# Kernel tuning notes

Hardware: AMD Instinct MI355X
Metric: run time of the kernel (lower is better)

The kernel has to match this reference:

```python
import jax, jax.numpy as jnp
import numpy as np

D = 32          # d_model / gcn channels
H_HEADS = 4
HEAD_D = D // H_HEADS
FF = 2048       # TransformerEncoderLayer default dim_feedforward
NUM_CLASSES = 10
EPS = 1e-5


def setup_inputs() -> dict:
    key = jax.random.key(0)
    ks = jax.random.split(key, 24)
    B, Cin, Hh, Ww = 1024, 16, 4, 8          # H*W == 32 (required by reshape into GCN)
    N = B * D                                 # 32768 graph nodes
    E = 2097152                               # ~avg degree 64
    p = lambda k, shp: (jax.random.normal(k, shp, dtype=jnp.float32) * 0.05)
    return {
        "x": jax.random.normal(ks[0], (B, Cin, Hh, Ww), dtype=jnp.float32),
        "edge_index": jax.random.randint(ks[1], (2, E), 0, N, dtype=jnp.int32),
        "conv_w": p(ks[2], (32, Cin, 3, 3)), "conv_b": p(ks[3], (32,)),
        "in_proj_w": p(ks[4], (3 * D, D)), "in_proj_b": p(ks[5], (3 * D,)),
        "out_proj_w": p(ks[6], (D, D)), "out_proj_b": p(ks[7], (D,)),
        "ln1_w": jnp.ones((D,), jnp.float32), "ln1_b": jnp.zeros((D,), jnp.float32),
        "ln2_w": jnp.ones((D,), jnp.float32), "ln2_b": jnp.zeros((D,), jnp.float32),
        "ff1_w": p(ks[8], (FF, D)), "ff1_b": p(ks[9], (FF,)),
        "ff2_w": p(ks[10], (D, FF)), "ff2_b": p(ks[11], (D,)),
        "gcn_w": p(ks[12], (D, D)), "gcn_b": p(ks[13], (D,)),
        "fc_w": p(ks[14], (NUM_CLASSES, D)), "fc_b": p(ks[15], (NUM_CLASSES,)),
    }


def _layernorm(v, w, b):
    m = v.mean(-1, keepdims=True)
    var = v.var(-1, keepdims=True)
    return (v - m) * jax.lax.rsqrt(var + EPS) * w + b


def _gcn(x, row, col, n, w, b):
    # PyG GCNConv: add self-loops, symmetric D^-1/2 (A+I) D^-1/2, x@W^T, + bias
    deg = jax.ops.segment_sum(jnp.ones(row.shape[0], x.dtype), col, num_segments=n)
    dis = jax.lax.rsqrt(jnp.maximum(deg, 1.0))  # self-loops guarantee deg>=1
    norm = dis[row] * dis[col]
    xw = x @ w.T
    msg = xw[row] * norm[:, None]
    return jax.ops.segment_sum(msg, col, num_segments=n) + b


def reference(x, edge_index, conv_w, conv_b, in_proj_w, in_proj_b, out_proj_w,
              out_proj_b, ln1_w, ln1_b, ln2_w, ln2_b, ff1_w, ff1_b, ff2_w, ff2_b,
              gcn_w, gcn_b, fc_w, fc_b):
    # conv2d, padding=1 stride=1 -> SAME
    h = jax.lax.conv_general_dilated(x, conv_w, (1, 1), "SAME",
                                     dimension_numbers=("NCHW", "OIHW", "NCHW"))
    h = h + conv_b[None, :, None, None]
    B, C, Hh, Ww = h.shape
    z = h.reshape(B, C, Hh * Ww).transpose(0, 2, 1)  # (B, HW, 32)

    # torch TransformerEncoderLayer, batch_first=False: axis0=seq(B), axis1=batch(HW)
    qkv = z @ in_proj_w.T + in_proj_b                 # (S, Nb, 3D)
    q, k, v = jnp.split(qkv, 3, axis=-1)
    S, Nb = z.shape[0], z.shape[1]
    rs = lambda t: t.reshape(S, Nb, H_HEADS, HEAD_D)
    q, k, v = rs(q), rs(k), rs(v)
    scores = jnp.einsum("snhd,tnhd->nhst", q, k) / np.sqrt(HEAD_D).astype(np.float32)
    attn = jax.nn.softmax(scores, axis=-1)
    o = jnp.einsum("nhst,tnhd->snhd", attn, v).reshape(S, Nb, D)
    o = o @ out_proj_w.T + out_proj_b
    z = _layernorm(z + o, ln1_w, ln1_b)               # post-norm (torch default)
    ff = jax.nn.relu(z @ ff1_w.T + ff1_b) @ ff2_w.T + ff2_b
    z = _layernorm(z + ff, ln2_w, ln2_b)

    # (B, HW, 32) -> (B, 32, HW) -> (B*32, HW) ; HW == 32 so GCN in_channels match
    g = z.transpose(0, 2, 1).reshape(B * C, Hh * Ww)
    n = g.shape[0]
    loops = jnp.arange(n, dtype=edge_index.dtype)
    row = jnp.concatenate([edge_index[0], loops])
    col = jnp.concatenate([edge_index[1], loops])
    g = _gcn(g, row, col, n, gcn_w, gcn_b)
    g = jax.nn.relu(g)  # dropout is identity in eval mode
    g = _gcn(g, row, col, n, gcn_w, gcn_b)            # shared weights (same module)
    logits = g @ fc_w.T + fc_b
    return jax.nn.log_softmax(logits, axis=1)
```

## Files before the change

### kernel.cpp

```cpp
#include <hip/hip_runtime.h>

#define NTOK 32768

__global__ __launch_bounds__(256) void conv_kernel(
    const float* __restrict__ x, const float* __restrict__ w,
    const float* __restrict__ bias, float* __restrict__ z) {
  __shared__ float xs[16 * 32];
  __shared__ float wsm[32 * 145];
  __shared__ float bs[32];
  int b = blockIdx.x, tid = threadIdx.x;
  const float* xb = x + b * 512;
  for (int i = tid; i < 512; i += 256) xs[i] = xb[i];
  for (int i = tid; i < 4608; i += 256) wsm[(i / 144) * 145 + (i % 144)] = w[i];
  if (tid < 32) bs[tid] = bias[tid];
  __syncthreads();
  #pragma unroll
  for (int r = 0; r < 4; ++r) {
    int oid = r * 256 + tid;
    int co = oid & 31, pos = oid >> 5;
    int y = pos >> 3, xx = pos & 7;
    float acc = bs[co];
    const float* wr = &wsm[co * 145];
    for (int ci = 0; ci < 16; ++ci) {
      #pragma unroll
      for (int ky = 0; ky < 3; ++ky) {
        int yy = y + ky - 1;
        if (yy < 0 || yy > 3) continue;
        #pragma unroll
        for (int kx = 0; kx < 3; ++kx) {
          int xc = xx + kx - 1;
          if (xc < 0 || xc > 7) continue;
          acc += xs[ci * 32 + yy * 8 + xc] * wr[ci * 9 + ky * 3 + kx];
        }
      }
    }
    z[(b * 32 + pos) * 32 + co] = acc;
  }
}

__global__ __launch_bounds__(256) void qkv_kernel(
    const float* __restrict__ z, const float* __restrict__ W,
    const float* __restrict__ bias, float* __restrict__ qt,
    float* __restrict__ kt, float* __restrict__ vt) {
  __shared__ float wsm[96 * 32];
  __shared__ float bs[96];
  int tid = threadIdx.x;
  for (int i = tid; i < 3072; i += 256) wsm[i] = W[i];
  if (tid < 96) bs[tid] = bias[tid];
  __syncthreads();
  int s = tid >> 3, bl = tid & 7;
  int b = blockIdx.x * 8 + bl;
  int token = b * 32 + s;
  float zr[32];
  const float4* zp = (const float4*)(z + token * 32);
  #pragma unroll
  for (int i = 0; i < 8; ++i) {
    float4 v = zp[i];
    zr[i * 4 + 0] = v.x; zr[i * 4 + 1] = v.y; zr[i * 4 + 2] = v.z; zr[i * 4 + 3] = v.w;
  }
  for (int part = 0; part < 3; ++part) {
    float* dst = part == 0 ? qt : (part == 1 ? kt : vt);
    for (int hh = 0; hh < 4; ++hh) {
      float out[8];
      #pragma unroll
      for (int j = 0; j < 8; ++j) {
        int jj = part * 32 + hh * 8 + j;
        float a = bs[jj];
        const float* wr = &wsm[jj * 32];
        #pragma unroll
        for (int k = 0; k < 32; ++k) a += zr[k] * wr[k];
        out[j] = a;
      }
      float4* p = (float4*)(dst + ((size_t)(s * 4 + hh) * 1024 + b) * 8);
      p[0] = make_float4(out[0], out[1], out[2], out[3]);
      p[1] = make_float4(out[4], out[5], out[6], out[7]);
    }
  }
}

__global__ __launch_bounds__(256) void attn_kernel(
    const float* __restrict__ qt, const float* __restrict__ kt,
    const float* __restrict__ vt, float* __restrict__ o) {
  __shared__ __align__(16) float Ks[1024 * 8];
  __shared__ __align__(16) float Vs[1024 * 8];
  int slab = blockIdx.x >> 2, qc = blockIdx.x & 3;
  int tid = threadIdx.x;
  const float4* kp = (const float4*)(kt + (size_t)slab * 8192);
  const float4* vp = (const float4*)(vt + (size_t)slab * 8192);
  float4* ksp = (float4*)Ks;
  float4* vsp = (float4*)Vs;
  for (int i = tid; i < 2048; i += 256) { ksp[i] = kp[i]; vsp[i] = vp[i]; }
  __syncthreads();
  int b = qc * 256 + tid;
  const float4* qp = (const float4*)(qt + ((size_t)slab * 1024 + b) * 8);
  float4 q0 = qp[0], q1 = qp[1];
  const float scale = 0.35355339059327373f;
  q0.x *= scale; q0.y *= scale; q0.z *= scale; q0.w *= scale;
  q1.x *= scale; q1.y *= scale; q1.z *= scale; q1.w *= scale;
  float m = -1e30f;
  for (int t = 0; t < 1024; ++t) {
    const float4* kk = (const float4*)&Ks[t * 8];
    float4 k0 = kk[0], k1 = kk[1];
    float s = q0.x * k0.x + q0.y * k0.y + q0.z * k0.z + q0.w * k0.w +
              q1.x * k1.x + q1.y * k1.y + q1.z * k1.z + q1.w * k1.w;
    m = fmaxf(m, s);
  }
  float l = 0.f;
  float a0 = 0, a1 = 0, a2 = 0, a3 = 0, a4 = 0, a5 = 0, a6 = 0, a7 = 0;
  for (int t = 0; t < 1024; ++t) {
    const float4* kk = (const float4*)&Ks[t * 8];
    float4 k0 = kk[0], k1 = kk[1];
    float s = q0.x * k0.x + q0.y * k0.y + q0.z * k0.z + q0.w * k0.w +
              q1.x * k1.x + q1.y * k1.y + q1.z * k1.z + q1.w * k1.w;
    float p = __expf(s - m);
    l += p;
    const float4* vv = (const float4*)&Vs[t * 8];
    float4 v0 = vv[0], v1 = vv[1];
    a0 += p * v0.x; a1 += p * v0.y; a2 += p * v0.z; a3 += p * v0.w;
    a4 += p * v1.x; a5 += p * v1.y; a6 += p * v1.z; a7 += p * v1.w;
  }
  float inv = 1.f / l;
  int npos = slab >> 2, hh = slab & 3;
  float4* op = (float4*)(o + ((size_t)(b * 32 + npos)) * 32 + hh * 8);
  op[0] = make_float4(a0 * inv, a1 * inv, a2 * inv, a3 * inv);
  op[1] = make_float4(a4 * inv, a5 * inv, a6 * inv, a7 * inv);
}

__global__ __launch_bounds__(256) void proj_ln1_kernel(
    const float* __restrict__ z, const float* __restrict__ o,
    const float* __restrict__ W, const float* __restrict__ bias,
    const float* __restrict__ lw, const float* __restrict__ lb,
    float* __restrict__ zn1) {
  __shared__ float wsm[1024];
  __shared__ float bs[32], lws[32], lbs[32];
  int tid = threadIdx.x;
  for (int i = tid; i < 1024; i += 256) wsm[i] = W[i];
  if (tid < 32) { bs[tid] = bias[tid]; lws[tid] = lw[tid]; lbs[tid] = lb[tid]; }
  __syncthreads();
  int token = blockIdx.x * 256 + tid;
  float orow[32], zrow[32], v[32];
  const float4* opnt = (const float4*)(o + (size_t)token * 32);
  const float4* zp = (const float4*)(z + (size_t)token * 32);
  #pragma unroll
  for (int i = 0; i < 8; ++i) {
    float4 t4 = opnt[i];
    orow[i * 4] = t4.x; orow[i * 4 + 1] = t4.y; orow[i * 4 + 2] = t4.z; orow[i * 4 + 3] = t4.w;
    float4 z4 = zp[i];
    zrow[i * 4] = z4.x; zrow[i * 4 + 1] = z4.y; zrow[i * 4 + 2] = z4.z; zrow[i * 4 + 3] = z4.w;
  }
  float s1 = 0.f, s2 = 0.f;
  for (int j = 0; j < 32; ++j) {
    float a = bs[j];
    const float* wr = &wsm[j * 32];
    #pragma unroll
    for (int k = 0; k < 32; ++k) a += orow[k] * wr[k];
    float t = a + zrow[j];
    v[j] = t; s1 += t; s2 += t * t;
  }
  float mean = s1 * (1.f / 32.f);
  float var = s2 * (1.f / 32.f) - mean * mean;
  float rs = rsqrtf(var + 1e-5f);
  float4* dst = (float4*)(zn1 + (size_t)token * 32);
  #pragma unroll
  for (int k4 = 0; k4 < 8; ++k4) {
    float4 ov;
    ov.x = (v[k4 * 4 + 0] - mean) * rs * lws[k4 * 4 + 0] + lbs[k4 * 4 + 0];
    ov.y = (v[k4 * 4 + 1] - mean) * rs * lws[k4 * 4 + 1] + lbs[k4 * 4 + 1];
    ov.z = (v[k4 * 4 + 2] - mean) * rs * lws[k4 * 4 + 2] + lbs[k4 * 4 + 2];
    ov.w = (v[k4 * 4 + 3] - mean) * rs * lws[k4 * 4 + 3] + lbs[k4 * 4 + 3];
    dst[k4] = ov;
  }
}

__global__ __launch_bounds__(256, 2) void ffn_kernel(
    const float* __restrict__ zn1, const float* __restrict__ w1,
    const float* __restrict__ b1, const float* __restrict__ w2,
    const float* __restrict__ b2, const float* __restrict__ lw,
    const float* __restrict__ lb, float* __restrict__ zn2) {
  __shared__ __align__(16) float zT[64 * 36];
  __shared__ float w1T[32 * 128];
  __shared__ __align__(16) float w2T[128 * 36];
  __shared__ __align__(16) float hT[64 * 132];
  __shared__ float b1s[128];
  __shared__ float lws[32], lbs[32], b2s[32];
  float* outT = hT;
  int tid = threadIdx.x;
  int t0 = blockIdx.x * 64;
  for (int i = tid; i < 512; i += 256) {
    int rw = i >> 3, c4 = i & 7;
    float4 v = ((const float4*)(zn1 + (size_t)(t0 + rw) * 32))[c4];
    *(float4*)&zT[rw * 36 + c4 * 4] = v;
  }
  if (tid < 32) { lws[tid] = lw[tid]; lbs[tid] = lb[tid]; b2s[tid] = b2[tid]; }
  __syncthreads();
  int tok4 = tid >> 2, dg = tid & 3;
  int f = tid & 127, hi = tid >> 7;
  float acc[8];
  #pragma unroll
  for (int j = 0; j < 8; ++j) acc[j] = b2s[dg * 8 + j];
  for (int ch = 0; ch < 16; ++ch) {
    __syncthreads();
    for (int i = tid; i < 1024; i += 256) {
      int fr = i & 127, k4 = i >> 7;
      float4 v = ((const float4*)(w1 + (size_t)(ch * 128 + fr) * 32))[k4];
      w1T[(k4 * 4 + 0) * 128 + fr] = v.x;
      w1T[(k4 * 4 + 1) * 128 + fr] = v.y;
      w1T[(k4 * 4 + 2) * 128 + fr] = v.z;
      w1T[(k4 * 4 + 3) * 128 + fr] = v.w;
    }
    for (int i = tid; i < 1024; i += 256) {
      int d = i & 31, f4 = i >> 5;
      float4 v = ((const float4*)(w2 + (size_t)d * 2048 + ch * 128))[f4];
      w2T[(f4 * 4 + 0) * 36 + d] = v.x;
      w2T[(f4 * 4 + 1) * 36 + d] = v.y;
      w2T[(f4 * 4 + 2) * 36 + d] = v.z;
      w2T[(f4 * 4 + 3) * 36 + d] = v.w;
    }
    if (tid < 128) b1s[tid] = b1[ch * 128 + tid];
    __syncthreads();
    float w1c[32];
    #pragma unroll
    for (int k = 0; k < 32; ++k) w1c[k] = w1T[k * 128 + f];
    float bb = b1s[f];
    for (int ii = 0; ii < 32; ++ii) {
      int tk = 2 * ii + hi;
      const float4* zr4 = (const float4*)&zT[tk * 36];
      float a = bb;
      #pragma unroll
      for (int k4 = 0; k4 < 8; ++k4) {
        float4 zv = zr4[k4];
        a += zv.x * w1c[k4 * 4] + zv.y * w1c[k4 * 4 + 1] + zv.z * w1c[k4 * 4 + 2] + zv.w * w1c[k4 * 4 + 3];
      }
      hT[tk * 132 + f] = fmaxf(a, 0.f);
    }
    __syncthreads();
    for (int fi = 0; fi < 128; ++fi) {
      float hv = hT[tok4 * 132 + fi];
      const float4* wr = (const float4*)&w2T[fi * 36 + dg * 8];
      float4 x0 = wr[0], x1 = wr[1];
      acc[0] += hv * x0.x; acc[1] += hv * x0.y; acc[2] += hv * x0.z; acc[3] += hv * x0.w;
      acc[4] += hv * x1.x; acc[5] += hv * x1.y; acc[6] += hv * x1.z; acc[7] += hv * x1.w;
    }
  }
  __syncthreads();
  #pragma unroll
  for (int j = 0; j < 8; ++j) outT[tok4 * 33 + dg * 8 + j] = acc[j];
  __syncthreads();
  if (tid < 64) {
    float v[32];
    float s1 = 0.f, s2 = 0.f;
    #pragma unroll
    for (int k = 0; k < 32; ++k) {
      float t = zT[tid * 36 + k] + outT[tid * 33 + k];
      v[k] = t; s1 += t; s2 += t * t;
    }
    float mean = s1 * (1.f / 32.f);
    float var = s2 * (1.f / 32.f) - mean * mean;
    float rs = rsqrtf(var + 1e-5f);
    float4* dst = (float4*)(zn2 + (size_t)(t0 + tid) * 32);
    #pragma unroll
    for (int k4 = 0; k4 < 8; ++k4) {
      float4 ov;
      ov.x = (v[k4 * 4 + 0] - mean) * rs * lws[k4 * 4 + 0] + lbs[k4 * 4 + 0];
      ov.y = (v[k4 * 4 + 1] - mean) * rs * lws[k4 * 4 + 1] + lbs[k4 * 4 + 1];
      ov.z = (v[k4 * 4 + 2] - mean) * rs * lws[k4 * 4 + 2] + lbs[k4 * 4 + 2];
      ov.w = (v[k4 * 4 + 3] - mean) * rs * lws[k4 * 4 + 3] + lbs[k4 * 4 + 3];
      dst[k4] = ov;
    }
  }
}

__global__ __launch_bounds__(256) void transpose_kernel(
    const float* __restrict__ zn2, float* __restrict__ g) {
  __shared__ float t[32 * 33];
  int b = blockIdx.x, tid = threadIdx.x;
  const float* src = zn2 + (size_t)b * 1024;
  #pragma unroll
  for (int l = 0; l < 4; ++l) {
    int o_ = l * 256 + tid;
    t[(o_ >> 5) * 33 + (o_ & 31)] = src[o_];
  }
  __syncthreads();
  float* dst = g + (size_t)b * 1024;
  #pragma unroll
  for (int l = 0; l < 4; ++l) {
    int o_ = l * 256 + tid;
    int c = o_ >> 5, s = o_ & 31;
    dst[o_] = t[s * 33 + c];
  }
}

__global__ void degi_kernel(const int* __restrict__ col, int* __restrict__ degi, int E) {
  int e = blockIdx.x * 256 + threadIdx.x;
  if (e < E) atomicAdd(&degi[col[e]], 1);
}

__global__ __launch_bounds__(1024) void scan_kernel(
    const int* __restrict__ degi, int* __restrict__ offs, int* __restrict__ cur,
    float* __restrict__ dis, int E) {
  __shared__ int ts[1024];
  int tid = threadIdx.x;
  int base = tid * 32;
  int loc[32];
  int s = 0;
  #pragma unroll
  for (int i = 0; i < 32; ++i) { loc[i] = s; s += degi[base + i]; }
  ts[tid] = s;
  __syncthreads();
  for (int d = 1; d < 1024; d <<= 1) {
    int v = (tid >= d) ? ts[tid - d] : 0;
    __syncthreads();
    ts[tid] += v;
    __syncthreads();
  }
  int excl = (tid == 0) ? 0 : ts[tid - 1];
  #pragma unroll
  for (int i = 0; i < 32; ++i) {
    int o = excl + loc[i];
    offs[base + i] = o;
    cur[base + i] = o;
    dis[base + i] = rsqrtf((float)(degi[base + i] + 1));
  }
  if (tid == 1023) offs[NTOK] = E;
}

__global__ void fill_kernel(const int* __restrict__ row, const int* __restrict__ col,
                            const float* __restrict__ dis, int* __restrict__ cur,
                            int2* __restrict__ erec, int E) {
  int e = blockIdx.x * 256 + threadIdx.x;
  if (e >= E) return;
  int r = row[e], c = col[e];
  int slot = atomicAdd(&cur[c], 1);
  float nrm = dis[r] * dis[c];
  erec[slot] = make_int2(r, __float_as_int(nrm));
}

__global__ __launch_bounds__(256) void gcn_in_kernel(
    const float* __restrict__ g, const float* __restrict__ w,
    float* __restrict__ xw) {
  __shared__ float wsm[1024];
  int tid = threadIdx.x;
  for (int i = tid; i < 1024; i += 256) wsm[i] = w[i];
  __syncthreads();
  int n = blockIdx.x * 256 + tid;
  float gr[32];
  const float4* gp = (const float4*)(g + (size_t)n * 32);
  #pragma unroll
  for (int i = 0; i < 8; ++i) {
    float4 v = gp[i];
    gr[i * 4] = v.x; gr[i * 4 + 1] = v.y; gr[i * 4 + 2] = v.z; gr[i * 4 + 3] = v.w;
  }
  float4* xp = (float4*)(xw + (size_t)n * 32);
  for (int d4 = 0; d4 < 8; ++d4) {
    float o_[4];
    #pragma unroll
    for (int j = 0; j < 4; ++j) {
      const float* wr = &wsm[(d4 * 4 + j) * 32];
      float a = 0.f;
      #pragma unroll
      for (int k = 0; k < 32; ++k) a += gr[k] * wr[k];
      o_[j] = a;
    }
    xp[d4] = make_float4(o_[0], o_[1], o_[2], o_[3]);
  }
}

__global__ __launch_bounds__(256) void gather_kernel(
    const float* __restrict__ xw, const float* __restrict__ dis,
    const int* __restrict__ offs, const int2* __restrict__ erec,
    float* __restrict__ agg) {
  int gid = blockIdx.x * 256 + threadIdx.x;
  int c = gid >> 3, q = gid & 7;
  int start = offs[c], end = offs[c + 1];
  float dn = dis[c];
  float dn2 = dn * dn;
  float4 self = ((const float4*)(xw + (size_t)c * 32))[q];
  float a0 = self.x * dn2, a1 = self.y * dn2, a2 = self.z * dn2, a3 = self.w * dn2;
  int e = start;
  #pragma unroll 4
  for (; e < end; ++e) {
    int2 rec = erec[e];
    float nrm = __int_as_float(rec.y);
    float4 v = ((const float4*)(xw + (size_t)rec.x * 32))[q];
    a0 += v.x * nrm; a1 += v.y * nrm; a2 += v.z * nrm; a3 += v.w * nrm;
  }
  ((float4*)(agg + (size_t)c * 32))[q] = make_float4(a0, a1, a2, a3);
}

__global__ __launch_bounds__(256) void gcn_mid_kernel(
    const float* __restrict__ agg, const float* __restrict__ gb,
    const float* __restrict__ w, float* __restrict__ xw2) {
  __shared__ float wsm[1024];
  __shared__ float bs[32];
  int tid = threadIdx.x;
  for (int i = tid; i < 1024; i += 256) wsm[i] = w[i];
  if (tid < 32) bs[tid] = gb[tid];
  __syncthreads();
  int n = blockIdx.x * 256 + tid;
  float gr[32];
  const float4* ap = (const float4*)(agg + (size_t)n * 32);
  #pragma unroll
  for (int i = 0; i < 8; ++i) {
    float4 v = ap[i];
    gr[i * 4 + 0] = fmaxf(v.x + bs[i * 4 + 0], 0.f);
    gr[i * 4 + 1] = fmaxf(v.y + bs[i * 4 + 1], 0.f);
    gr[i * 4 + 2] = fmaxf(v.z + bs[i * 4 + 2], 0.f);
    gr[i * 4 + 3] = fmaxf(v.w + bs[i * 4 + 3], 0.f);
  }
  float4* xp = (float4*)(xw2 + (size_t)n * 32);
  for (int d4 = 0; d4 < 8; ++d4) {
    float o_[4];
    #pragma unroll
    for (int j = 0; j < 4; ++j) {
      const float* wr = &wsm[(d4 * 4 + j) * 32];
      float a = 0.f;
      #pragma unroll
      for (int k = 0; k < 32; ++k) a += gr[k] * wr[k];
      o_[j] = a;
    }
    xp[d4] = make_float4(o_[0], o_[1], o_[2], o_[3]);
  }
}

__global__ __launch_bounds__(256) void gcn_out_kernel(
    const float* __restrict__ agg2, const float* __restrict__ gb,
    const float* __restrict__ fw, const float* __restrict__ fb,
    float* __restrict__ out) {
  __shared__ float wsm[320];
  __shared__ float bs[10];
  __shared__ float gbs[32];
  int tid = threadIdx.x;
  for (int i = tid; i < 320; i += 256) wsm[i] = fw[i];
  if (tid < 10) bs[tid] = fb[tid];
  if (tid < 32) gbs[tid] = gb[tid];
  __syncthreads();
  int n = blockIdx.x * 256 + tid;
  float v[32];
  const float4* ap = (const float4*)(agg2 + (size_t)n * 32);
  #pragma unroll
  for (int i = 0; i < 8; ++i) {
    float4 t4 = ap[i];
    v[i * 4 + 0] = t4.x + gbs[i * 4 + 0];
    v[i * 4 + 1] = t4.y + gbs[i * 4 + 1];
    v[i * 4 + 2] = t4.z + gbs[i * 4 + 2];
    v[i * 4 + 3] = t4.w + gbs[i * 4 + 3];
  }
  float lg[10];
  float mx = -1e30f;
  for (int j = 0; j < 10; ++j) {
    float a = bs[j];
    const float* wr = &wsm[j * 32];
    #pragma unroll
    for (int k = 0; k < 32; ++k) a += v[k] * wr[k];
    lg[j] = a;
    mx = fmaxf(mx, a);
  }
  float se = 0.f;
  for (int j = 0; j < 10; ++j) se += __expf(lg[j] - mx);
  float ls = logf(se);
  for (int j = 0; j < 10; ++j) out[(size_t)n * 10 + j] = lg[j] - mx - ls;
}

extern "C" void kernel_launch(void* const* d_in, const int* in_sizes, int n_in,
                              void* d_out, int out_size, void* d_ws, size_t ws_size,
                              hipStream_t stream) {
  const float* x      = (const float*)d_in[0];
  const int*   ei     = (const int*)d_in[1];
  const float* conv_w = (const float*)d_in[2];
  const float* conv_b = (const float*)d_in[3];
  const float* in_w   = (const float*)d_in[4];
  const float* in_b   = (const float*)d_in[5];
  const float* out_w  = (const float*)d_in[6];
  const float* out_b  = (const float*)d_in[7];
  const float* ln1_w  = (const float*)d_in[8];
  const float* ln1_b  = (const float*)d_in[9];
  const float* ln2_w  = (const float*)d_in[10];
  const float* ln2_b  = (const float*)d_in[11];
  const float* ff1_w  = (const float*)d_in[12];
  const float* ff1_b  = (const float*)d_in[13];
  const float* ff2_w  = (const float*)d_in[14];
  const float* ff2_b  = (const float*)d_in[15];
  const float* gcn_w  = (const float*)d_in[16];
  const float* gcn_b  = (const float*)d_in[17];
  const float* fc_w   = (const float*)d_in[18];
  const float* fc_b   = (const float*)d_in[19];
  int E = in_sizes[1] / 2;
  const int* rowp = ei;
  const int* colp = ei + E;

  float* wsf = (float*)d_ws;
  const size_t M = 1048576;
  float* Z   = wsf + 0 * M;
  float* QT  = wsf + 1 * M;
  float* KT  = wsf + 2 * M;
  float* VT  = wsf + 3 * M;
  float* O   = wsf + 4 * M;
  float* ZN1 = wsf + 5 * M;
  float* ZN2 = wsf + 6 * M;
  int*   DEGI = (int*)(wsf + 7 * M);
  int*   OFFS = DEGI + 32768;
  int*   CUR  = OFFS + 32770;
  float* DIS  = (float*)(CUR + 32768);
  int2*  EREC = (int2*)(DIS + 32768);
  float* G   = QT;
  float* XW  = KT;
  float* AGG = VT;
  float* XW2 = O;
  float* AG2 = Z;

  conv_kernel<<<1024, 256, 0, stream>>>(x, conv_w, conv_b, Z);
  qkv_kernel<<<128, 256, 0, stream>>>(Z, in_w, in_b, QT, KT, VT);
  attn_kernel<<<512, 256, 0, stream>>>(QT, KT, VT, O);
  proj_ln1_kernel<<<128, 256, 0, stream>>>(Z, O, out_w, out_b, ln1_w, ln1_b, ZN1);
  ffn_kernel<<<512, 256, 0, stream>>>(ZN1, ff1_w, ff1_b, ff2_w, ff2_b, ln2_w, ln2_b, ZN2);
  transpose_kernel<<<1024, 256, 0, stream>>>(ZN2, G);
  hipMemsetAsync(DEGI, 0, 32768 * sizeof(int), stream);
  degi_kernel<<<(E + 255) / 256, 256, 0, stream>>>(colp, DEGI, E);
  scan_kernel<<<1, 1024, 0, stream>>>(DEGI, OFFS, CUR, DIS, E);
  fill_kernel<<<(E + 255) / 256, 256, 0, stream>>>(rowp, colp, DIS, CUR, EREC, E);
  gcn_in_kernel<<<128, 256, 0, stream>>>(G, gcn_w, XW);
  gather_kernel<<<1024, 256, 0, stream>>>(XW, DIS, OFFS, EREC, AGG);
  gcn_mid_kernel<<<128, 256, 0, stream>>>(AGG, gcn_b, gcn_w, XW2);
  gather_kernel<<<1024, 256, 0, stream>>>(XW2, DIS, OFFS, EREC, AG2);
  gcn_out_kernel<<<128, 256, 0, stream>>>(AG2, gcn_b, fc_w, fc_b, (float*)d_out);
}
```

Before: 813.1 us.

## Restructure FFN kernel to register-resident tokens with split-F shuffle reduction

The FFN kernel now keeps two tokens' inputs and full 32-wide output accumulators in registers per thread. Each group of 8 lanes splits the 128-feature chunk, computes the hidden activation and immediately accumulates the second matmul, then reduces across lanes with xor shuffles. This drops the hidden-activation shared buffer and one barrier per chunk, cutting LDS traffic. The cost is heavy register pressure (over 128 accumulator and input floats per thread), which may lower occupancy or cause spills, and only 1 in 8 lanes does the final layernorm.

```diff
diff --git a/kernel.cpp b/kernel.cpp
--- a/kernel.cpp
+++ b/kernel.cpp
@@ -177,87 +177,111 @@
     const float* __restrict__ b1, const float* __restrict__ w2,
     const float* __restrict__ b2, const float* __restrict__ lw,
     const float* __restrict__ lb, float* __restrict__ zn2) {
-  __shared__ __align__(16) float zT[64 * 36];
-  __shared__ float w1T[32 * 128];
-  __shared__ __align__(16) float w2T[128 * 36];
-  __shared__ __align__(16) float hT[64 * 132];
+  __shared__ __align__(16) float w1s[128 * 36];
+  __shared__ __align__(16) float w2s[128 * 36];
   __shared__ float b1s[128];
   __shared__ float lws[32], lbs[32], b2s[32];
-  float* outT = hT;
-  int tid = threadIdx.x;
-  int t0 = blockIdx.x * 64;
-  for (int i = tid; i < 512; i += 256) {
-    int rw = i >> 3, c4 = i & 7;
-    float4 v = ((const float4*)(zn1 + (size_t)(t0 + rw) * 32))[c4];
-    *(float4*)&zT[rw * 36 + c4 * 4] = v;
-  }
+  int tid = threadIdx.x;
+  int p = tid >> 3, fg = tid & 7;
+  int t0 = blockIdx.x * 64 + p * 2;
+  float z0[32], z1[32], acc0[32], acc1[32];
+  const float4* zp0 = (const float4*)(zn1 + (size_t)t0 * 32);
+  const float4* zp1 = (const float4*)(zn1 + (size_t)(t0 + 1) * 32);
+  #pragma unroll
+  for (int i = 0; i < 8; ++i) {
+    float4 a = zp0[i];
+    z0[i * 4 + 0] = a.x; z0[i * 4 + 1] = a.y; z0[i * 4 + 2] = a.z; z0[i * 4 + 3] = a.w;
+    float4 b = zp1[i];
+    z1[i * 4 + 0] = b.x; z1[i * 4 + 1] = b.y; z1[i * 4 + 2] = b.z; z1[i * 4 + 3] = b.w;
+  }
+  #pragma unroll
+  for (int d = 0; d < 32; ++d) { acc0[d] = 0.f; acc1[d] = 0.f; }
   if (tid < 32) { lws[tid] = lw[tid]; lbs[tid] = lb[tid]; b2s[tid] = b2[tid]; }
-  __syncthreads();
-  int tok4 = tid >> 2, dg = tid & 3;
-  int f = tid & 127, hi = tid >> 7;
-  float acc[8];
-  #pragma unroll
-  for (int j = 0; j < 8; ++j) acc[j] = b2s[dg * 8 + j];
   for (int ch = 0; ch < 16; ++ch) {
     __syncthreads();
-    for (int i = tid; i < 1024; i += 256) {
-      int fr = i & 127, k4 = i >> 7;
+    #pragma unroll
+    for (int pass = 0; pass < 4; ++pass) {
+      int idx = pass * 256 + tid;
+      int fr = idx >> 3, k4 = idx & 7;
       float4 v = ((const float4*)(w1 + (size_t)(ch * 128 + fr) * 32))[k4];
-      w1T[(k4 * 4 + 0) * 128 + fr] = v.x;
-      w1T[(k4 * 4 + 1) * 128 + fr] = v.y;
-      w1T[(k4 * 4 + 2) * 128 + fr] = v.z;
-      w1T[(k4 * 4 + 3) * 128 + fr] = v.w;
-    }
-    for (int i = tid; i < 1024; i += 256) {
-      int d = i & 31, f4 = i >> 5;
-      float4 v = ((const float4*)(w2 + (size_t)d * 2048 + ch * 128))[f4];
-      w2T[(f4 * 4 + 0) * 36 + d] = v.x;
-      w2T[(f4 * 4 + 1) * 36 + d] = v.y;
-      w2T[(f4 * 4 + 2) * 36 + d] = v.z;
-      w2T[(f4 * 4 + 3) * 36 + d] = v.w;
+      float* dptr = &w1s[fr * 36 + k4 * 4];
+      dptr[0] = v.x; dptr[1] = v.y; dptr[2] = v.z; dptr[3] = v.w;
+    }
+    #pragma unroll
+    for (int pass = 0; pass < 4; ++pass) {
+      int idx = pass * 256 + tid;
+      int dd = idx >> 5, f4 = idx & 31;
+      float4 v = ((const float4*)(w2 + (size_t)dd * 2048 + ch * 128))[f4];
+      w2s[(f4 * 4 + 0) * 36 + dd] = v.x;
+      w2s[(f4 * 4 + 1) * 36 + dd] = v.y;
+      w2s[(f4 * 4 + 2) * 36 + dd] = v.z;
+      w2s[(f4 * 4 + 3) * 36 + dd] = v.w;
     }
     if (tid < 128) b1s[tid] = b1[ch * 128 + tid];
     __syncthreads();
-    float w1c[32];
-    #pragma unroll
-    for (int k = 0; k < 32; ++k) w1c[k] = w1T[k * 128 + f];
-    float bb = b1s[f];
-    for (int ii = 0; ii < 32; ++ii) {
-      int tk = 2 * ii + hi;
-      const float4* zr4 = (const float4*)&zT[tk * 36];
-      float a = bb;
+    #pragma unroll 4
+    for (int i = 0; i < 16; ++i) {
+      int f = i * 8 + fg;
+      const float4* wr = (const float4*)&w1s[f * 36];
+      float h0 = b1s[f], h1 = h0;
       #pragma unroll
       for (int k4 = 0; k4 < 8; ++k4) {
-        float4 zv = zr4[k4];
-        a += zv.x * w1c[k4 * 4] + zv.y * w1c[k4 * 4 + 1] + zv.z * w1c[k4 * 4 + 2] + zv.w * w1c[k4 * 4 + 3];
+        float4 wv = wr[k4];
+        h0 += z0[k4 * 4 + 0] * wv.x + z0[k4 * 4 + 1] * wv.y + z0[k4 * 4 + 2] * wv.z + z0[k4 * 4 + 3] * wv.w;
+        h1 += z1[k4 * 4 + 0] * wv.x + z1[k4 * 4 + 1] * wv.y + z1[k4 * 4 + 2] * wv.z + z1[k4 * 4 + 3] * wv.w;
       }
-      hT[tk * 132 + f] = fmaxf(a, 0.f);
-    }
-    __syncthreads();
-    for (int fi = 0; fi < 128; ++fi) {
-      float hv = hT[tok4 * 132 + fi];
-      const float4* wr = (const float4*)&w2T[fi * 36 + dg * 8];
-      float4 x0 = wr[0], x1 = wr[1];
-      acc[0] += hv * x0.x; acc[1] += hv * x0.y; acc[2] += hv * x0.z; acc[3] += hv * x0.w;
-      acc[4] += hv * x1.x; acc[5] += hv * x1.y; acc[6] += hv * x1.z; acc[7] += hv * x1.w;
-    }
-  }
-  __syncthreads();
-  #pragma unroll
-  for (int j = 0; j < 8; ++j) outT[tok4 * 33 + dg * 8 + j] = acc[j];
-  __syncthreads();
-  if (tid < 64) {
+      h0 = fmaxf(h0, 0.f); h1 = fmaxf(h1, 0.f);
+      const float4* vr = (const float4*)&w2s[f * 36];
+      #pragma unroll
+      for (int d4 = 0; d4 < 8; ++d4) {
+        float4 vv = vr[d4];
+        acc0[d4 * 4 + 0] += h0 * vv.x; acc0[d4 * 4 + 1] += h0 * vv.y;
+        acc0[d4 * 4 + 2] += h0 * vv.z; acc0[d4 * 4 + 3] += h0 * vv.w;
+        acc1[d4 * 4 + 0] += h1 * vv.x; acc1[d4 * 4 + 1] += h1 * vv.y;
+        acc1[d4 * 4 + 2] += h1 * vv.z; acc1[d4 * 4 + 3] += h1 * vv.w;
+      }
+    }
+  }
+  #pragma unroll
+  for (int d = 0; d < 32; ++d) {
+    float a = acc0[d];
+    a += __shfl_xor(a, 1); a += __shfl_xor(a, 2); a += __shfl_xor(a, 4);
+    acc0[d] = a;
+    float b = acc1[d];
+    b += __shfl_xor(b, 1); b += __shfl_xor(b, 2); b += __shfl_xor(b, 4);
+    acc1[d] = b;
+  }
+  if (fg == 0) {
     float v[32];
     float s1 = 0.f, s2 = 0.f;
     #pragma unroll
-    for (int k = 0; k < 32; ++k) {
-      float t = zT[tid * 36 + k] + outT[tid * 33 + k];
-      v[k] = t; s1 += t; s2 += t * t;
+    for (int d = 0; d < 32; ++d) {
+      float t = z0[d] + acc0[d] + b2s[d];
+      v[d] = t; s1 += t; s2 += t * t;
     }
     float mean = s1 * (1.f / 32.f);
     float var = s2 * (1.f / 32.f) - mean * mean;
     float rs = rsqrtf(var + 1e-5f);
-    float4* dst = (float4*)(zn2 + (size_t)(t0 + tid) * 32);
+    float4* dst = (float4*)(zn2 + (size_t)t0 * 32);
+    #pragma unroll
+    for (int k4 = 0; k4 < 8; ++k4) {
+      float4 ov;
+      ov.x = (v[k4 * 4 + 0] - mean) * rs * lws[k4 * 4 + 0] + lbs[k4 * 4 + 0];
+      ov.y = (v[k4 * 4 + 1] - mean) * rs * lws[k4 * 4 + 1] + lbs[k4 * 4 + 1];
+      ov.z = (v[k4 * 4 + 2] - mean) * rs * lws[k4 * 4 + 2] + lbs[k4 * 4 + 2];
+      ov.w = (v[k4 * 4 + 3] - mean) * rs * lws[k4 * 4 + 3] + lbs[k4 * 4 + 3];
+      dst[k4] = ov;
+    }
+    float s1b = 0.f, s2b = 0.f;
+    #pragma unroll
+    for (int d = 0; d < 32; ++d) {
+      float t = z1[d] + acc1[d] + b2s[d];
+      v[d] = t; s1b += t; s2b += t * t;
+    }
+    mean = s1b * (1.f / 32.f);
+    var = s2b * (1.f / 32.f) - mean * mean;
+    rs = rsqrtf(var + 1e-5f);
+    dst = (float4*)(zn2 + (size_t)(t0 + 1) * 32);
     #pragma unroll
     for (int k4 = 0; k4 < 8; ++k4) {
       float4 ov;
```

Result: no change. 800.3 us (-1.6%).
